# Optimization experiments

Hardware: AMD Instinct MI355X
Metric: run time of the kernel (lower is better)

Reference implementation:

```python
import jax, jax.numpy as jnp
import numpy as np

V, D, H, L, F, S, B = 32000, 1024, 16, 4, 4096, 1024, 2
THETA = 10000.0
EPS = 1e-5


def rmsnorm(x, w):
    # faithful to source: rms = sqrt(mean(x^2)) + eps (eps OUTSIDE the sqrt)
    rms = jnp.sqrt(jnp.mean(x * x, axis=-1, keepdims=True)) + EPS
    return (x / rms) * w


def rope(x, pos):
    # x: [B, H, S, dk]; rotate interleaved even/odd pairs
    dk = x.shape[-1]
    inv_freq = 1.0 / (THETA ** (jnp.arange(0, dk, 2, dtype=jnp.float32) / dk))
    ang = pos[:, None].astype(jnp.float32) * inv_freq[None, :]  # [S, dk/2]
    cos, sin = jnp.cos(ang), jnp.sin(ang)
    x1, x2 = x[..., ::2], x[..., 1::2]
    r1 = x1 * cos - x2 * sin
    r2 = x1 * sin + x2 * cos
    return jnp.stack([r1, r2], axis=-1).reshape(x.shape)


def setup_inputs() -> dict:
    key = jax.random.key(0)
    ks = jax.random.split(key, 12)
    s_attn = np.sqrt(2.0 / (D + D)).astype(np.float32)
    s_ffn = np.sqrt(2.0 / (F + D)).astype(np.float32)
    s_head = np.sqrt(2.0 / (V + D)).astype(np.float32)
    return {
        "token_ids": jax.random.randint(ks[0], (B, S), 0, V),
        "tok_emb": jax.random.normal(ks[1], (V, D), jnp.float32),
        "lm_head_w": jax.random.normal(ks[2], (V, D), jnp.float32) * s_head,
        "ln_final_w": jnp.ones((D,), jnp.float32),
        "q_w": jax.random.normal(ks[3], (L, D, D), jnp.float32) * s_attn,
        "k_w": jax.random.normal(ks[4], (L, D, D), jnp.float32) * s_attn,
        "v_w": jax.random.normal(ks[5], (L, D, D), jnp.float32) * s_attn,
        "o_w": jax.random.normal(ks[6], (L, D, D), jnp.float32) * s_attn,
        "ln1_w": jnp.ones((L, D), jnp.float32),
        "ln2_w": jnp.ones((L, D), jnp.float32),
        "w1": jax.random.normal(ks[7], (L, F, D), jnp.float32) * s_ffn,
        "w2": jax.random.normal(ks[8], (L, D, F), jnp.float32) * s_ffn,
        "w3": jax.random.normal(ks[9], (L, F, D), jnp.float32) * s_ffn,
    }


def reference(token_ids, tok_emb, lm_head_w, ln_final_w, q_w, k_w, v_w, o_w,
              ln1_w, ln2_w, w1, w2, w3):
    b, s = token_ids.shape
    dk = D // H
    scale = 1.0 / np.sqrt(dk).astype(np.float32)
    pos = jnp.arange(s)
    causal = jnp.tril(jnp.ones((s, s), dtype=bool))  # mask[i,j] = i >= j
    x = tok_emb[token_ids]  # [B, S, D]

    for l in range(L):
        # attention block with RoPE
        h = rmsnorm(x, ln1_w[l])
        q = (h @ q_w[l].T).reshape(b, s, H, dk).transpose(0, 2, 1, 3)
        k = (h @ k_w[l].T).reshape(b, s, H, dk).transpose(0, 2, 1, 3)
        v = (h @ v_w[l].T).reshape(b, s, H, dk).transpose(0, 2, 1, 3)
        q = rope(q, pos)
        k = rope(k, pos)
        scores = jnp.einsum('bhqd,bhkd->bhqk', q, k) * scale
        scores = jnp.where(causal, scores, -jnp.inf)
        attn = jax.nn.softmax(scores, axis=-1)
        o = jnp.einsum('bhqk,bhkd->bhqd', attn, v)
        o = o.transpose(0, 2, 1, 3).reshape(b, s, D)
        x = x + o @ o_w[l].T

        # SwiGLU FFN block
        h2 = rmsnorm(x, ln2_w[l])
        xw = h2 @ w1[l].T                       # [B, S, F]
        swish = xw * jax.nn.sigmoid(xw)
        x = x + (swish * (h2 @ w3[l].T)) @ w2[l].T

    x = rmsnorm(x, ln_final_w)
    return x @ lm_head_w.T  # logits [B, S, V]
```

## Files before the change

kernel.cpp:

```cpp
#include <hip/hip_runtime.h>
#include <math.h>

#define V_SZ 32000
#define D_SZ 1024
#define H_SZ 16
#define L_SZ 4
#define F_SZ 4096
#define S_SZ 1024
#define B_SZ 2
#define DK 64
#define NTOK (B_SZ * S_SZ)
#define NEG_INF -3.0e38f

typedef _Float16 half8 __attribute__((ext_vector_type(8)));
typedef _Float16 half4 __attribute__((ext_vector_type(4)));
typedef float floatx4 __attribute__((ext_vector_type(4)));

__device__ __forceinline__ void gload16(const void* g, void* l) {
    __builtin_amdgcn_global_load_lds(
        (const __attribute__((address_space(1))) unsigned int*)g,
        (__attribute__((address_space(3))) unsigned int*)l, 16, 0, 0);
}

__global__ __launch_bounds__(256) void prep1(const float* __restrict__ x,
                                             const float* __restrict__ lnw,
                                             _Float16* __restrict__ hout,
                                             const float* __restrict__ sq,
                                             const float* __restrict__ sk,
                                             const float* __restrict__ sv,
                                             const float* __restrict__ so,
                                             const float* __restrict__ s1,
                                             const float* __restrict__ s3,
                                             const float* __restrict__ s2,
                                             _Float16* __restrict__ d,
                                             int nDD8, int nFD8) {
    const int tid = threadIdx.x;
    if (blockIdx.x < NTOK) {
        const int row = blockIdx.x;
        const float4 v = ((const float4*)(x + (size_t)row * D_SZ))[tid];
        float ss = v.x * v.x + v.y * v.y + v.z * v.z + v.w * v.w;
#pragma unroll
        for (int off = 32; off > 0; off >>= 1) ss += __shfl_down(ss, off, 64);
        __shared__ float red[4];
        if ((tid & 63) == 0) red[tid >> 6] = ss;
        __syncthreads();
        const float tot = red[0] + red[1] + red[2] + red[3];
        const float inv = 1.0f / (sqrtf(tot * (1.0f / (float)D_SZ)) + 1e-5f);
        const float4 wv = ((const float4*)lnw)[tid];
        half4 o = {(_Float16)(v.x * inv * wv.x), (_Float16)(v.y * inv * wv.y),
                   (_Float16)(v.z * inv * wv.z), (_Float16)(v.w * inv * wv.w)};
        ((half4*)(hout + (size_t)row * D_SZ))[tid] = o;
        return;
    }
    const int i = (blockIdx.x - NTOK) * 256 + tid;
    const float* s;
    int off;
    if (i < 4 * nDD8) {
        const int sel = i / nDD8;
        off = i - sel * nDD8;
        s = sel == 0 ? sq : (sel == 1 ? sk : (sel == 2 ? sv : so));
    } else {
        const int j = i - 4 * nDD8;
        const int sel = j / nFD8;
        off = j - sel * nFD8;
        s = sel == 0 ? s1 : (sel == 1 ? s3 : s2);
    }
    const float4 a = ((const float4*)s)[2 * off];
    const float4 b = ((const float4*)s)[2 * off + 1];
    half8 hv = {(_Float16)a.x, (_Float16)a.y, (_Float16)a.z, (_Float16)a.w,
                (_Float16)b.x, (_Float16)b.y, (_Float16)b.z, (_Float16)b.w};
    ((half8*)d)[i] = hv;
}

__global__ __launch_bounds__(256) void prep2(const float* __restrict__ x,
                                             const float* __restrict__ lnw,
                                             _Float16* __restrict__ hout,
                                             const float* __restrict__ win,
                                             _Float16* __restrict__ wout) {
    const int tid = threadIdx.x;
    if (blockIdx.x < NTOK) {
        const int row = blockIdx.x;
        const float4 v = ((const float4*)(x + (size_t)row * D_SZ))[tid];
        float ss = v.x * v.x + v.y * v.y + v.z * v.z + v.w * v.w;
#pragma unroll
        for (int off = 32; off > 0; off >>= 1) ss += __shfl_down(ss, off, 64);
        __shared__ float red[4];
        if ((tid & 63) == 0) red[tid >> 6] = ss;
        __syncthreads();
        const float tot = red[0] + red[1] + red[2] + red[3];
        const float inv = 1.0f / (sqrtf(tot * (1.0f / (float)D_SZ)) + 1e-5f);
        const float4 wv = ((const float4*)lnw)[tid];
        half4 o = {(_Float16)(v.x * inv * wv.x), (_Float16)(v.y * inv * wv.y),
                   (_Float16)(v.z * inv * wv.z), (_Float16)(v.w * inv * wv.w)};
        ((half4*)(hout + (size_t)row * D_SZ))[tid] = o;
        return;
    }
    const int i = (blockIdx.x - NTOK) * 256 + tid;
    const float4 a = ((const float4*)win)[2 * i];
    const float4 b = ((const float4*)win)[2 * i + 1];
    half8 hv = {(_Float16)a.x, (_Float16)a.y, (_Float16)a.z, (_Float16)a.w,
                (_Float16)b.x, (_Float16)b.y, (_Float16)b.z, (_Float16)b.w};
    ((half8*)wout)[i] = hv;
}

__global__ __launch_bounds__(256) void embed_kernel(const int* __restrict__ ids,
                                                    const float* __restrict__ emb,
                                                    float* __restrict__ x) {
    const int row = blockIdx.x;
    const int id = ids[row];
    const float4* src = (const float4*)(emb + (size_t)id * D_SZ);
    float4* dst = (float4*)(x + (size_t)row * D_SZ);
    dst[threadIdx.x] = src[threadIdx.x];
}

__global__ __launch_bounds__(256) void rmsnorm_kernel(const float* __restrict__ x,
                                                      const float* __restrict__ w,
                                                      _Float16* __restrict__ out) {
    const int row = blockIdx.x;
    const int tid = threadIdx.x;
    const float4 v = ((const float4*)(x + (size_t)row * D_SZ))[tid];
    float ss = v.x * v.x + v.y * v.y + v.z * v.z + v.w * v.w;
#pragma unroll
    for (int off = 32; off > 0; off >>= 1) ss += __shfl_down(ss, off, 64);
    __shared__ float red[4];
    if ((tid & 63) == 0) red[tid >> 6] = ss;
    __syncthreads();
    const float tot = red[0] + red[1] + red[2] + red[3];
    const float inv = 1.0f / (sqrtf(tot * (1.0f / (float)D_SZ)) + 1e-5f);
    const float4 wv = ((const float4*)w)[tid];
    half4 o = {(_Float16)(v.x * inv * wv.x), (_Float16)(v.y * inv * wv.y),
               (_Float16)(v.z * inv * wv.z), (_Float16)(v.w * inv * wv.w)};
    ((half4*)(out + (size_t)row * D_SZ))[tid] = o;
}

template <bool MFAST>
__global__ __launch_bounds__(512) void hgemm8p(const _Float16* __restrict__ A,
                                               const _Float16* __restrict__ B,
                                               float* __restrict__ Cf,
                                               int M, int N, int K) {
    __shared__ __align__(16) _Float16 As[2][2][256 * 32];
    __shared__ __align__(16) _Float16 Bs[2][2][256 * 32];
    const int tid = threadIdx.x;
    const int lane = tid & 63, wave = tid >> 6;
    const int wm = wave >> 2, wn = wave & 3;
    const int l15 = lane & 15, g = lane >> 4;

    const int gm = M >> 8, gn = N >> 8, nwg = gm * gn;
    const int orig = blockIdx.x;
    const int q8 = nwg >> 3, r8 = nwg & 7, xcd = orig & 7, j8 = orig >> 3;
    const int wgid = (xcd < r8 ? xcd * (q8 + 1) : r8 * (q8 + 1) + (xcd - r8) * q8) + j8;
    const int bm = MFAST ? (wgid % gm) : (wgid / gn);
    const int bn = MFAST ? (wgid / gm) : (wgid % gn);
    const int m0 = bm << 8, n0 = bn << 8;

    const int rowS = tid >> 2;
    const int srcC = ((tid & 3) ^ ((rowS >> 1) & 3)) << 4;
    const size_t Kb = (size_t)K * 2;
    const char* gA = (const char*)A + (size_t)(m0 + rowS) * Kb + srcC;
    const char* gB = (const char*)B + (size_t)(n0 + rowS) * Kb + srcC;
    const size_t g128 = 128 * Kb;

#define STA(ks, t, buf) do {                                              \
        const char* _s = gA + (size_t)(t) * 128 + (ks) * 64;              \
        char* _d = (char*)&As[buf][ks][0];                                \
        gload16(_s, _d + tid * 16);                                       \
        gload16(_s + g128, _d + 8192 + tid * 16);                         \
    } while (0)
#define STB(ks, t, buf) do {                                              \
        const char* _s = gB + (size_t)(t) * 128 + (ks) * 64;              \
        char* _d = (char*)&Bs[buf][ks][0];                                \
        gload16(_s, _d + tid * 16);                                       \
        gload16(_s + g128, _d + 8192 + tid * 16);                         \
    } while (0)

    half8 aF[8], bF[2];
#define READA(buf, ks) do {                                               \
        _Pragma("unroll")                                                 \
        for (int i = 0; i < 8; i++) {                                     \
            const int R = wm * 128 + i * 16 + l15;                        \
            aF[i] = *(const half8*)((const char*)&As[buf][ks][0] +        \
                                    R * 64 + ((g ^ ((R >> 1) & 3)) << 4));\
        }                                                                 \
    } while (0)
#define READB(buf, ks, nh) do {                                           \
        _Pragma("unroll")                                                 \
        for (int jj = 0; jj < 2; jj++) {                                  \
            const int R = wn * 64 + ((nh) * 2 + jj) * 16 + l15;           \
            bF[jj] = *(const half8*)((const char*)&Bs[buf][ks][0] +       \
                                     R * 64 + ((g ^ ((R >> 1) & 3)) << 4));\
        }                                                                 \
    } while (0)
#define MFMA16(nh) do {                                                   \
        __builtin_amdgcn_s_setprio(1);                                    \
        _Pragma("unroll")                                                 \
        for (int i = 0; i < 8; i++) {                                     \
            acc[i][(nh) * 2 + 0] = __builtin_amdgcn_mfma_f32_16x16x32_f16(\
                aF[i], bF[0], acc[i][(nh) * 2 + 0], 0, 0, 0);             \
            acc[i][(nh) * 2 + 1] = __builtin_amdgcn_mfma_f32_16x16x32_f16(\
                aF[i], bF[1], acc[i][(nh) * 2 + 1], 0, 0, 0);             \
        }                                                                 \
        __builtin_amdgcn_s_setprio(0);                                    \
    } while (0)
#define FENCE_MID() do {                                                  \
        __builtin_amdgcn_s_barrier();                                     \
        asm volatile("s_waitcnt lgkmcnt(0)" ::: "memory");                \
        __builtin_amdgcn_sched_barrier(0);                                \
    } while (0)

    floatx4 acc[8][4];
#pragma unroll
    for (int i = 0; i < 8; i++)
#pragma unroll
        for (int j = 0; j < 4; j++) acc[i][j] = 0;

    const int nt = K >> 6;
    STA(0, 0, 0); STB(0, 0, 0); STA(1, 0, 0); STB(1, 0, 0);
    STA(0, 1, 1); STB(0, 1, 1);

    for (int t = 0; t < nt; ++t) {
        const int buf = t & 1, nbuf = buf ^ 1;
        if (t == nt - 1) asm volatile("s_waitcnt vmcnt(0)" ::: "memory");
        else             asm volatile("s_waitcnt vmcnt(4)" ::: "memory");
        __builtin_amdgcn_s_barrier();
        READA(buf, 0); READB(buf, 0, 0);
        if (t + 1 < nt) STA(1, t + 1, nbuf);
        FENCE_MID();
        MFMA16(0);
        __builtin_amdgcn_s_barrier();
        READB(buf, 0, 1);
        if (t + 1 < nt) STB(1, t + 1, nbuf);
        FENCE_MID();
        MFMA16(1);
        __builtin_amdgcn_s_barrier();
        READA(buf, 1); READB(buf, 1, 0);
        if (t + 2 < nt) STA(0, t + 2, buf);
        FENCE_MID();
        MFMA16(0);
        __builtin_amdgcn_s_barrier();
        READB(buf, 1, 1);
        if (t + 2 < nt) STB(0, t + 2, buf);
        FENCE_MID();
        MFMA16(1);
        __builtin_amdgcn_s_barrier();
    }
#undef STA
#undef STB
#undef READA
#undef READB
#undef MFMA16
#undef FENCE_MID

#pragma unroll
    for (int i = 0; i < 8; i++) {
#pragma unroll
        for (int e = 0; e < 4; e++) {
            const int row = m0 + wm * 128 + i * 16 + g * 4 + e;
#pragma unroll
            for (int j = 0; j < 4; j++) {
                const int col = n0 + wn * 64 + j * 16 + l15;
                Cf[(size_t)row * N + col] = acc[i][j][e];
            }
        }
    }
}

template <int EPI, bool MFAST, int TM>
__global__ __launch_bounds__(256) void hgemm(const _Float16* __restrict__ A,
                                             const _Float16* __restrict__ B,
                                             float* __restrict__ Cf,
                                             _Float16* Ch,
                                             const _Float16* AUXh,
                                             _Float16* Cq,
                                             _Float16* Ck,
                                             _Float16* Cv,
                                             int M, int N, int K) {
    constexpr int WN = (TM == 128) ? 2 : 4;
    constexpr int CW = 128 / WN;
    constexpr int FN = CW / 16;
    __shared__ __align__(16) _Float16 As[2][TM * 32];
    __shared__ __align__(16) _Float16 Bs[2][128 * 32];
    const int tid = threadIdx.x;
    const int lane = tid & 63;
    const int wave = tid >> 6;
    const int wr = (TM == 128) ? (wave >> 1) : 0;
    const int wc = (TM == 128) ? (wave & 1) : wave;
    const int l15 = lane & 15, g = lane >> 4;

    const int gm = M / TM, gn = N >> 7, nwg = gm * gn;
    const int orig = blockIdx.x;
    const int q8 = nwg >> 3, r8 = nwg & 7, xcd = orig & 7, j8 = orig >> 3;
    const int wgid = (xcd < r8 ? xcd * (q8 + 1) : r8 * (q8 + 1) + (xcd - r8) * q8) + j8;
    const int bm = MFAST ? (wgid % gm) : (wgid / gn);
    const int bn = MFAST ? (wgid / gm) : (wgid % gn);
    const int m0 = bm * TM, n0 = bn * 128;

    const int offA0 = wave * (TM * 16) + lane * 16;
    const int offA1 = offA0 + 1024;
    const int rA0 = offA0 >> 6, kA0 = offA0 & 63;
    const int rA1 = offA1 >> 6, kA1 = offA1 & 63;
    const int offB0 = wave * 2048 + lane * 16;
    const int offB1 = offB0 + 1024;
    const int rB0 = offB0 >> 6, kB0 = offB0 & 63;
    const int rB1 = offB1 >> 6, kB1 = offB1 & 63;
    const char* gA0 = (const char*)(A + (size_t)(m0 + rA0) * K) + kA0;
    const char* gA1 = (const char*)(A + (size_t)(m0 + rA1) * K) + kA1;
    const char* gB0 = (const char*)(B + (size_t)(n0 + rB0) * K) + kB0;
    const char* gB1 = (const char*)(B + (size_t)(n0 + rB1) * K) + kB1;

#define STAGE(buf)                                                     \
    do {                                                               \
        gload16(gA0, (char*)As[buf] + offA0);                          \
        if constexpr (TM == 128) gload16(gA1, (char*)As[buf] + offA1); \
        gload16(gB0, (char*)Bs[buf] + offB0);                          \
        gload16(gB1, (char*)Bs[buf] + offB1);                          \
        gA0 += 64; gA1 += 64; gB0 += 64; gB1 += 64;                    \
    } while (0)

    floatx4 acc[4][FN];
#pragma unroll
    for (int i = 0; i < 4; i++)
#pragma unroll
        for (int j = 0; j < FN; j++) acc[i][j] = 0;

    STAGE(0);
    __syncthreads();
    int cur = 0;
    for (int kk = 0; kk < K; kk += 32) {
        if (kk + 32 < K) STAGE(cur ^ 1);
        half8 aF[4], bF[FN];
#pragma unroll
        for (int i = 0; i < 4; i++)
            aF[i] = *(const half8*)&As[cur][(wr * 64 + i * 16 + l15) * 32 + g * 8];
#pragma unroll
        for (int j = 0; j < FN; j++)
            bF[j] = *(const half8*)&Bs[cur][(wc * CW + j * 16 + l15) * 32 + g * 8];
#pragma unroll
        for (int i = 0; i < 4; i++)
#pragma unroll
            for (int j = 0; j < FN; j++)
                acc[i][j] = __builtin_amdgcn_mfma_f32_16x16x32_f16(aF[i], bF[j], acc[i][j], 0, 0, 0);
        __syncthreads();
        cur ^= 1;
    }
#undef STAGE

    const int rb = m0 + wr * 64 + g * 4;
    const int cb = n0 + wc * CW + l15;
    if (EPI == 4) {
        const int sel = n0 >> 10;
        _Float16* Cx = sel == 0 ? Cq : (sel == 1 ? Ck : Cv);
        const int cb0 = cb - sel * 1024;
#pragma unroll
        for (int i = 0; i < 4; i++) {
#pragma unroll
            for (int e = 0; e < 4; e++) {
                const int row = rb + i * 16 + e;
                const int pos = row & (S_SZ - 1);
#pragma unroll
                for (int j = 0; j < FN; j++) {
                    float v = acc[i][j][e];
                    const int col = cb0 + j * 16;
                    if (sel < 2) {
                        const float pp = __shfl_xor(v, 1, 64);
                        const int pi = (col & 63) >> 1;
                        const float invf = exp2f((float)pi * -0.41524101186f);
                        float sn, cs;
                        sincosf((float)pos * invf, &sn, &cs);
                        v = (col & 1) ? (pp * sn + v * cs) : (v * cs - pp * sn);
                    }
                    Cx[(size_t)row * 1024 + col] = (_Float16)v;
                }
            }
        }
        return;
    }
#pragma unroll
    for (int i = 0; i < 4; i++) {
#pragma unroll
        for (int e = 0; e < 4; e++) {
            const int row = rb + i * 16 + e;
#pragma unroll
            for (int j = 0; j < FN; j++) {
                const float v = acc[i][j][e];
                const int col = cb + j * 16;
                if (EPI == 0) {
                    Cf[(size_t)row * N + col] = v;
                } else if (EPI == 1) {
                    Cf[(size_t)row * N + col] += v;
                } else if (EPI == 2) {
                    Ch[(size_t)row * N + col] =
                        (_Float16)(v / (1.0f + __expf(-v)));
                } else if (EPI == 3) {
                    const size_t idx = (size_t)row * N + col;
                    Ch[idx] = (_Float16)((float)AUXh[idx] * v);
                }
            }
        }
    }
}

__global__ __launch_bounds__(256) void hgemm_ff(const _Float16* __restrict__ A,
                                                const _Float16* __restrict__ B1,
                                                const _Float16* __restrict__ B3,
                                                _Float16* __restrict__ Ch,
                                                int M, int N, int K) {
    __shared__ __align__(16) _Float16 As[2][64 * 32];
    __shared__ __align__(16) _Float16 Bs1[2][128 * 32];
    __shared__ __align__(16) _Float16 Bs3[2][128 * 32];
    const int tid = threadIdx.x;
    const int lane = tid & 63;
    const int wave = tid >> 6;
    const int l15 = lane & 15, g = lane >> 4;

    const int gm = M >> 6, gn = N >> 7, nwg = gm * gn;
    const int orig = blockIdx.x;
    const int q8 = nwg >> 3, r8 = nwg & 7, xcd = orig & 7, j8 = orig >> 3;
    const int wgid = (xcd < r8 ? xcd * (q8 + 1) : r8 * (q8 + 1) + (xcd - r8) * q8) + j8;
    const int bm = wgid % gm, bn = wgid / gm;
    const int m0 = bm * 64, n0 = bn * 128;

    const int offA = wave * 1024 + lane * 16;
    const int rA = offA >> 6, kA = offA & 63;
    const int offB0 = wave * 2048 + lane * 16;
    const int offB1 = offB0 + 1024;
    const int rB0 = offB0 >> 6, kB0 = offB0 & 63;
    const int rB1 = offB1 >> 6, kB1 = offB1 & 63;
    const char* gA  = (const char*)(A  + (size_t)(m0 + rA) * K) + kA;
    const char* gB10 = (const char*)(B1 + (size_t)(n0 + rB0) * K) + kB0;
    const char* gB11 = (const char*)(B1 + (size_t)(n0 + rB1) * K) + kB1;
    const char* gB30 = (const char*)(B3 + (size_t)(n0 + rB0) * K) + kB0;
    const char* gB31 = (const char*)(B3 + (size_t)(n0 + rB1) * K) + kB1;

#define STAGEF(buf)                                   \
    do {                                              \
        gload16(gA,   (char*)As[buf]  + offA);        \
        gload16(gB10, (char*)Bs1[buf] + offB0);       \
        gload16(gB11, (char*)Bs1[buf] + offB1);       \
        gload16(gB30, (char*)Bs3[buf] + offB0);       \
        gload16(gB31, (char*)Bs3[buf] + offB1);       \
        gA += 64; gB10 += 64; gB11 += 64;             \
        gB30 += 64; gB31 += 64;                       \
    } while (0)

    floatx4 acc1[4][2], acc3[4][2];
#pragma unroll
    for (int i = 0; i < 4; i++)
#pragma unroll
        for (int j = 0; j < 2; j++) { acc1[i][j] = 0; acc3[i][j] = 0; }

    STAGEF(0);
    __syncthreads();
    int cur = 0;
    for (int kk = 0; kk < K; kk += 32) {
        if (kk + 32 < K) STAGEF(cur ^ 1);
        half8 aF[4], b1F[2], b3F[2];
#pragma unroll
        for (int i = 0; i < 4; i++)
            aF[i] = *(const half8*)&As[cur][(i * 16 + l15) * 32 + g * 8];
#pragma unroll
        for (int j = 0; j < 2; j++) {
            b1F[j] = *(const half8*)&Bs1[cur][(wave * 32 + j * 16 + l15) * 32 + g * 8];
            b3F[j] = *(const half8*)&Bs3[cur][(wave * 32 + j * 16 + l15) * 32 + g * 8];
        }
#pragma unroll
        for (int i = 0; i < 4; i++)
#pragma unroll
            for (int j = 0; j < 2; j++) {
                acc1[i][j] = __builtin_amdgcn_mfma_f32_16x16x32_f16(aF[i], b1F[j], acc1[i][j], 0, 0, 0);
                acc3[i][j] = __builtin_amdgcn_mfma_f32_16x16x32_f16(aF[i], b3F[j], acc3[i][j], 0, 0, 0);
            }
        __syncthreads();
        cur ^= 1;
    }
#undef STAGEF

    const int cb = n0 + wave * 32 + l15;
#pragma unroll
    for (int i = 0; i < 4; i++) {
#pragma unroll
        for (int e = 0; e < 4; e++) {
            const int row = m0 + i * 16 + g * 4 + e;
#pragma unroll
            for (int j = 0; j < 2; j++) {
                const float v1 = acc1[i][j][e];
                const float v3 = acc3[i][j][e];
                const float sw = v1 / (1.0f + __expf(-v1));
                Ch[(size_t)row * N + cb + j * 16] = (_Float16)(sw * v3);
            }
        }
    }
}

__global__ __launch_bounds__(256) void vtrans(const _Float16* __restrict__ vh,
                                              _Float16* __restrict__ vt) {
    __shared__ __align__(16) _Float16 Ls[64][80];
    const int t = threadIdx.x;
    const int s0 = blockIdx.x * 64;
    const int bh = blockIdx.y;
    const int b = bh >> 4, h = bh & 15;
#pragma unroll
    for (int p = 0; p < 2; ++p) {
        const int sl = p * 32 + (t >> 3);
        const int d = (t & 7) * 8;
        *(half8*)&Ls[sl][d] =
            *(const half8*)&vh[((size_t)b * S_SZ + s0 + sl) * D_SZ + h * 64 + d];
    }
    __syncthreads();
#pragma unroll
    for (int p = 0; p < 2; ++p) {
        const int d = p * 32 + (t >> 3);
        const int sc = (t & 7) * 8;
        half8 v;
#pragma unroll
        for (int j = 0; j < 8; ++j) v[j] = Ls[sc + j][d];
        *(half8*)&vt[((size_t)bh * 64 + d) * S_SZ + s0 + sc] = v;
    }
}

__global__ __launch_bounds__(256) void attn_split(const _Float16* __restrict__ qh,
                                                  const _Float16* __restrict__ kh,
                                                  const _Float16* __restrict__ vt,
                                                  _Float16* __restrict__ aop,
                                                  float2* __restrict__ ml) {
    __shared__ __align__(16) _Float16 Ks[2][64 * 64];
    __shared__ __align__(16) _Float16 Vs[2][64 * 64];
    __shared__ __align__(16) _Float16 Ps[4][16][88];
    const int tid = threadIdx.x;
    const int lane = tid & 63, wave = tid >> 6;
    const int l15 = lane & 15, g = lane >> 4;
    const int bx = blockIdx.x;
    const int bh = blockIdx.y;
    const int par = blockIdx.z;
    const int h = bh & 15;
    const size_t tokb = (size_t)(bh >> 4) * S_SZ;

    const int qt0 = bx, qt1 = 15 - bx;
    const int qb0 = qt0 * 64, qb1 = qt1 * 64;
    const int ktmax = qt1;

    const int qrow = l15 * 4 + wave;
    half8 qA0[2], qA1[2];
#pragma unroll
    for (int kk = 0; kk < 2; ++kk) {
        qA0[kk] = *(const half8*)&qh[(tokb + qb0 + qrow) * D_SZ + h * 64 + kk * 32 + g * 8];
        qA1[kk] = *(const half8*)&qh[(tokb + qb1 + qrow) * D_SZ + h * 64 + kk * 32 + g * 8];
    }

    floatx4 accO0[4], accO1[4];
#pragma unroll
    for (int s = 0; s < 4; s++) { accO0[s] = 0; accO1[s] = 0; }
    float m0_[4] = {NEG_INF, NEG_INF, NEG_INF, NEG_INF};
    float l0_[4] = {0.0f, 0.0f, 0.0f, 0.0f};
    float m1_[4] = {NEG_INF, NEG_INF, NEG_INF, NEG_INF};
    float l1_[4] = {0.0f, 0.0f, 0.0f, 0.0f};

    const char* KbB = (const char*)(kh + tokb * D_SZ + h * 64);
    const char* VbB = (const char*)(vt + (size_t)bh * 64 * S_SZ);
    const int so0 = wave * 2048 + lane * 16;
    const int so1 = so0 + 1024;
    const int r0 = so0 >> 7, c0 = (so0 >> 4) & 7;
    const int r1 = so1 >> 7, c1 = (so1 >> 4) & 7;
    const int gc0 = ((c0 ^ (r0 & 7)) << 4);
    const int gc1 = ((c1 ^ (r1 & 7)) << 4);

#define STAGEKV(buf, kt)                                                   \
    do {                                                                   \
        const size_t kvr = (size_t)(kt) * 64;                              \
        gload16(KbB + (kvr + r0) * 2048 + gc0, (char*)Ks[buf] + so0);      \
        gload16(KbB + (kvr + r1) * 2048 + gc1, (char*)Ks[buf] + so1);      \
        gload16(VbB + r0 * 2048 + kvr * 2 + gc0, (char*)Vs[buf] + so0);    \
        gload16(VbB + r1 * 2048 + kvr * 2 + gc1, (char*)Vs[buf] + so1);    \
    } while (0)

#define LDSW(arr, rr, cc) \
    (*(const half8*)&(arr)[(rr) * 64 + ((((cc) ^ ((rr) & 7))) << 3)])

    auto computeTile = [&](const half8* qA, floatx4* accO, float* m_, float* l_,
                           int qbase, int kt, bool diag, int buf) {
        const int kv0 = kt * 64;
        floatx4 accS[4];
        __builtin_amdgcn_s_setprio(1);
#pragma unroll
        for (int sub = 0; sub < 4; ++sub) {
            accS[sub] = 0;
#pragma unroll
            for (int kk = 0; kk < 2; ++kk) {
                half8 kB = LDSW(Ks[buf], sub * 16 + l15, kk * 4 + g);
                accS[sub] = __builtin_amdgcn_mfma_f32_16x16x32_f16(qA[kk], kB, accS[sub], 0, 0, 0);
            }
        }
        __builtin_amdgcn_s_setprio(0);
        float sv[4][4];
        float mx[4] = {NEG_INF, NEG_INF, NEG_INF, NEG_INF};
#pragma unroll
        for (int sub = 0; sub < 4; ++sub)
#pragma unroll
            for (int e = 0; e < 4; ++e) {
                float s = accS[sub][e] * 0.125f;
                if (diag && (kv0 + sub * 16 + l15 > qbase + (g * 4 + e) * 4 + wave))
                    s = NEG_INF;
                sv[sub][e] = s;
                mx[e] = fmaxf(mx[e], s);
            }
#pragma unroll
        for (int msk = 1; msk <= 8; msk <<= 1)
#pragma unroll
            for (int e = 0; e < 4; ++e)
                mx[e] = fmaxf(mx[e], __shfl_xor(mx[e], msk, 64));
        float sf[4];
#pragma unroll
        for (int e = 0; e < 4; ++e) {
            const float mn = fmaxf(m_[e], mx[e]);
            sf[e] = __expf(m_[e] - mn);
            m_[e] = mn;
        }
        float rs[4] = {0.0f, 0.0f, 0.0f, 0.0f};
#pragma unroll
        for (int sub = 0; sub < 4; ++sub)
#pragma unroll
            for (int e = 0; e < 4; ++e) {
                const float p = __expf(sv[sub][e] - m_[e]);
                sv[sub][e] = p;
                rs[e] += p;
            }
#pragma unroll
        for (int msk = 1; msk <= 8; msk <<= 1)
#pragma unroll
            for (int e = 0; e < 4; ++e)
                rs[e] += __shfl_xor(rs[e], msk, 64);
#pragma unroll
        for (int e = 0; e < 4; ++e) l_[e] = l_[e] * sf[e] + rs[e];
#pragma unroll
        for (int sub = 0; sub < 4; ++sub)
#pragma unroll
            for (int e = 0; e < 4; ++e) accO[sub][e] *= sf[e];
#pragma unroll
        for (int sub = 0; sub < 4; ++sub)
#pragma unroll
            for (int e = 0; e < 4; ++e)
                Ps[wave][g * 4 + e][sub * 16 + l15] = (_Float16)sv[sub][e];
        half8 aP[2];
        aP[0] = *(const half8*)&Ps[wave][l15][g * 8];
        aP[1] = *(const half8*)&Ps[wave][l15][32 + g * 8];
        __builtin_amdgcn_s_setprio(1);
#pragma unroll
        for (int sub = 0; sub < 4; ++sub)
#pragma unroll
            for (int kk = 0; kk < 2; ++kk) {
                half8 vB = LDSW(Vs[buf], sub * 16 + l15, kk * 4 + g);
                accO[sub] = __builtin_amdgcn_mfma_f32_16x16x32_f16(aP[kk], vB, accO[sub], 0, 0, 0);
            }
        __builtin_amdgcn_s_setprio(0);
    };

    STAGEKV(0, par);
    __syncthreads();
    int cur = 0;
    for (int kt = par; kt <= ktmax; kt += 2) {
        if (kt + 2 <= ktmax) STAGEKV(cur ^ 1, kt + 2);
        computeTile(qA1, accO1, m1_, l1_, qb1, kt, kt == qt1, cur);
        if (kt <= qt0)
            computeTile(qA0, accO0, m0_, l0_, qb0, kt, kt == qt0, cur);
        __syncthreads();
        cur ^= 1;
    }
#undef STAGEKV
#undef LDSW

    _Float16* op = aop + (size_t)par * ((size_t)NTOK * D_SZ);
    float2* mlp = ml + (size_t)par * (B_SZ * H_SZ * S_SZ);
#pragma unroll
    for (int e = 0; e < 4; ++e) {
        const int rr = (g * 4 + e) * 4 + wave;
        const float i1 = l1_[e] > 0.0f ? 1.0f / l1_[e] : 0.0f;
        const float i0 = l0_[e] > 0.0f ? 1.0f / l0_[e] : 0.0f;
#pragma unroll
        for (int sub = 0; sub < 4; ++sub) {
            op[(tokb + qb1 + rr) * D_SZ + h * 64 + sub * 16 + l15] =
                (_Float16)(accO1[sub][e] * i1);
            op[(tokb + qb0 + rr) * D_SZ + h * 64 + sub * 16 + l15] =
                (_Float16)(accO0[sub][e] * i0);
        }
        if (l15 == 0) {
            mlp[bh * S_SZ + qb1 + rr] = float2{m1_[e], l1_[e]};
            mlp[bh * S_SZ + qb0 + rr] = float2{m0_[e], l0_[e]};
        }
    }
}

__global__ __launch_bounds__(256) void attn_merge(const _Float16* __restrict__ aop,
                                                  const float2* __restrict__ ml,
                                                  _Float16* __restrict__ ao) {
    const int row = blockIdx.x;
    const int t = threadIdx.x;
    const int col = t * 4;
    const int h = col >> 6;
    const int b = row >> 10, s = row & (S_SZ - 1);
    const int bh = b * H_SZ + h;
    const float2 v0 = ml[bh * S_SZ + s];
    const float2 v1 = ml[B_SZ * H_SZ * S_SZ + bh * S_SZ + s];
    const float m = fmaxf(v0.x, v1.x);
    const float w0 = v0.y * __expf(v0.x - m);
    const float w1 = v1.y * __expf(v1.x - m);
    const float inv = 1.0f / (w0 + w1);
    const float a0 = w0 * inv, a1 = w1 * inv;
    const size_t base = (size_t)row * D_SZ + col;
    const half4 x0 = *(const half4*)(aop + base);
    const half4 x1 = *(const half4*)(aop + (size_t)NTOK * D_SZ + base);
    half4 o;
#pragma unroll
    for (int j = 0; j < 4; ++j)
        o[j] = (_Float16)(a0 * (float)x0[j] + a1 * (float)x1[j]);
    *(half4*)(ao + base) = o;
}

extern "C" void kernel_launch(void* const* d_in, const int* in_sizes, int n_in,
                              void* d_out, int out_size, void* d_ws, size_t ws_size,
                              hipStream_t stream) {
    const int*   token_ids  = (const int*)d_in[0];
    const float* tok_emb    = (const float*)d_in[1];
    const float* lm_head_w  = (const float*)d_in[2];
    const float* ln_final_w = (const float*)d_in[3];
    const float* q_w        = (const float*)d_in[4];
    const float* k_w        = (const float*)d_in[5];
    const float* v_w        = (const float*)d_in[6];
    const float* o_w        = (const float*)d_in[7];
    const float* ln1_w      = (const float*)d_in[8];
    const float* ln2_w      = (const float*)d_in[9];
    const float* w1         = (const float*)d_in[10];
    const float* w2         = (const float*)d_in[11];
    const float* w3         = (const float*)d_in[12];
    float* out = (float*)d_out;

    char* W = (char*)d_ws;
    const size_t MB = 1u << 20;
    float*    x    = (float*)(W + 0);
    _Float16* h    = (_Float16*)(W + 8 * MB);
    _Float16* ao   = (_Float16*)(W + 12 * MB);
    _Float16* wq   = (_Float16*)(W + 16 * MB);
    _Float16* wo   = wq + 3 * (1u << 20);
    _Float16* ww1  = (_Float16*)(W + 24 * MB);
    _Float16* ww3  = ww1 + (size_t)F_SZ * D_SZ;
    _Float16* ww2  = ww1 + 2 * (size_t)F_SZ * D_SZ;
    _Float16* qh   = (_Float16*)(W + 48 * MB);
    _Float16* kh   = (_Float16*)(W + 52 * MB);
    _Float16* vh   = (_Float16*)(W + 56 * MB);
    _Float16* vt   = (_Float16*)(W + 60 * MB);
    _Float16* ff1h = (_Float16*)(W + 64 * MB);
    _Float16* aop  = (_Float16*)(W + 64 * MB);
    float2*   ml   = (float2*)(W + 72 * MB);
    _Float16* whead = (_Float16*)(W + 24 * MB);

    embed_kernel<<<NTOK, 256, 0, stream>>>(token_ids, tok_emb, x);

    const int nDD8 = D_SZ * D_SZ / 8;
    const int nFD8 = F_SZ * D_SZ / 8;
    const int nCNV = 4 * nDD8 + 3 * nFD8;
    const dim3 gPRE1(NTOK + nCNV / 256);
    const dim3 gQKV(3 * D_SZ / 128 * (NTOK / 128));
    const dim3 gD64(D_SZ / 128 * (NTOK / 64));
    const dim3 gFF(F_SZ / 128 * (NTOK / 64));
    const dim3 gATT(S_SZ / 128, B_SZ * H_SZ, 2);
    const dim3 gVT(S_SZ / 64, B_SZ * H_SZ);

    for (int l = 0; l < L_SZ; l++) {
        const size_t oDD = (size_t)l * D_SZ * D_SZ;
        const size_t oFD = (size_t)l * F_SZ * D_SZ;
        prep1<<<gPRE1, 256, 0, stream>>>(x, ln1_w + (size_t)l * D_SZ, h,
                                         q_w + oDD, k_w + oDD, v_w + oDD, o_w + oDD,
                                         w1 + oFD, w3 + oFD, w2 + oFD,
                                         wq, nDD8, nFD8);
        hgemm<4, true, 128><<<gQKV, 256, 0, stream>>>(h, wq, nullptr, nullptr, nullptr,
                                                      qh, kh, vh, NTOK, 3 * D_SZ, D_SZ);
        vtrans<<<gVT, 256, 0, stream>>>(vh, vt);
        attn_split<<<gATT, 256, 0, stream>>>(qh, kh, vt, aop, ml);
        attn_merge<<<NTOK, 256, 0, stream>>>(aop, ml, ao);
        hgemm<1, false, 64><<<gD64, 256, 0, stream>>>(ao, wo, x, nullptr, nullptr,
                                                      nullptr, nullptr, nullptr, NTOK, D_SZ, D_SZ);
        rmsnorm_kernel<<<NTOK, 256, 0, stream>>>(x, ln2_w + (size_t)l * D_SZ, h);
        hgemm_ff<<<gFF, 256, 0, stream>>>(h, ww1, ww3, ff1h, NTOK, F_SZ, D_SZ);
        hgemm<1, false, 64><<<gD64, 256, 0, stream>>>(ff1h, ww2, x, nullptr, nullptr,
                                                      nullptr, nullptr, nullptr, NTOK, D_SZ, F_SZ);
    }
    const int nVD8 = V_SZ * D_SZ / 8;
    prep2<<<NTOK + nVD8 / 256, 256, 0, stream>>>(x, ln_final_w, h, lm_head_w, whead);
    const dim3 gOUT(V_SZ / 256 * (NTOK / 256));
    hgemm8p<true><<<gOUT, 512, 0, stream>>>(h, whead, out, NTOK, V_SZ, D_SZ);
}
```

Before: 1.182 ms.

## Split-K residual GEMMs with atomics, fuse V transpose into QKV epilogue

The two residual-add GEMMs (o_proj and w2) now use split-K=2 with atomicAdd into the fp32 residual, doubling the number of workgroups. The QKV GEMM epilogue writes V directly in transposed [b,h,d,s] layout, which removes the separate vtrans kernel and its round trip through memory. The QKV GEMM also moves from 128-row to 64-row tiles to get more workgroups. The costs are float atomic traffic, nondeterministic summation order, and strided scattered stores for V.

```diff
diff --git a/kernel.cpp b/kernel.cpp
--- a/kernel.cpp
+++ b/kernel.cpp
@@ -264,7 +264,7 @@
     }
 }
 
-template <int EPI, bool MFAST, int TM>
+template <int EPI, bool MFAST, int TM, int SPLITK>
 __global__ __launch_bounds__(256) void hgemm(const _Float16* __restrict__ A,
                                              const _Float16* __restrict__ B,
                                              float* __restrict__ Cf,
@@ -286,13 +286,17 @@
     const int wc = (TM == 128) ? (wave & 1) : wave;
     const int l15 = lane & 15, g = lane >> 4;
 
-    const int gm = M / TM, gn = N >> 7, nwg = gm * gn;
+    const int gm = M / TM, gn = N >> 7, nwgT = gm * gn * SPLITK;
     const int orig = blockIdx.x;
-    const int q8 = nwg >> 3, r8 = nwg & 7, xcd = orig & 7, j8 = orig >> 3;
+    const int q8 = nwgT >> 3, r8 = nwgT & 7, xcd = orig & 7, j8 = orig >> 3;
     const int wgid = (xcd < r8 ? xcd * (q8 + 1) : r8 * (q8 + 1) + (xcd - r8) * q8) + j8;
-    const int bm = MFAST ? (wgid % gm) : (wgid / gn);
-    const int bn = MFAST ? (wgid / gm) : (wgid % gn);
+    const int sk = wgid % SPLITK;
+    const int tile = wgid / SPLITK;
+    const int bm = MFAST ? (tile % gm) : (tile / gn);
+    const int bn = MFAST ? (tile / gm) : (tile % gn);
     const int m0 = bm * TM, n0 = bn * 128;
+    const int Kh = K / SPLITK;
+    const int kOff = sk * Kh * 2;
 
     const int offA0 = wave * (TM * 16) + lane * 16;
     const int offA1 = offA0 + 1024;
@@ -302,10 +306,10 @@
     const int offB1 = offB0 + 1024;
     const int rB0 = offB0 >> 6, kB0 = offB0 & 63;
     const int rB1 = offB1 >> 6, kB1 = offB1 & 63;
-    const char* gA0 = (const char*)(A + (size_t)(m0 + rA0) * K) + kA0;
-    const char* gA1 = (const char*)(A + (size_t)(m0 + rA1) * K) + kA1;
-    const char* gB0 = (const char*)(B + (size_t)(n0 + rB0) * K) + kB0;
-    const char* gB1 = (const char*)(B + (size_t)(n0 + rB1) * K) + kB1;
+    const char* gA0 = (const char*)(A + (size_t)(m0 + rA0) * K) + kA0 + kOff;
+    const char* gA1 = (const char*)(A + (size_t)(m0 + rA1) * K) + kA1 + kOff;
+    const char* gB0 = (const char*)(B + (size_t)(n0 + rB0) * K) + kB0 + kOff;
+    const char* gB1 = (const char*)(B + (size_t)(n0 + rB1) * K) + kB1 + kOff;
 
 #define STAGE(buf)                                                     \
     do {                                                               \
@@ -325,8 +329,8 @@
     STAGE(0);
     __syncthreads();
     int cur = 0;
-    for (int kk = 0; kk < K; kk += 32) {
-        if (kk + 32 < K) STAGE(cur ^ 1);
+    for (int kk = 0; kk < Kh; kk += 32) {
+        if (kk + 32 < Kh) STAGE(cur ^ 1);
         half8 aF[4], bF[FN];
 #pragma unroll
         for (int i = 0; i < 4; i++)
@@ -348,7 +352,6 @@
     const int cb = n0 + wc * CW + l15;
     if (EPI == 4) {
         const int sel = n0 >> 10;
-        _Float16* Cx = sel == 0 ? Cq : (sel == 1 ? Ck : Cv);
         const int cb0 = cb - sel * 1024;
 #pragma unroll
         for (int i = 0; i < 4; i++) {
@@ -367,8 +370,12 @@
                         float sn, cs;
                         sincosf((float)pos * invf, &sn, &cs);
                         v = (col & 1) ? (pp * sn + v * cs) : (v * cs - pp * sn);
+                        _Float16* Cx = sel == 0 ? Cq : Ck;
+                        Cx[(size_t)row * 1024 + col] = (_Float16)v;
+                    } else {
+                        Cv[(((size_t)(row >> 10) << 10) + col) * S_SZ +
+                           (row & (S_SZ - 1))] = (_Float16)v;
                     }
-                    Cx[(size_t)row * 1024 + col] = (_Float16)v;
                 }
             }
         }
@@ -386,7 +393,8 @@
                 if (EPI == 0) {
                     Cf[(size_t)row * N + col] = v;
                 } else if (EPI == 1) {
-                    Cf[(size_t)row * N + col] += v;
+                    if (SPLITK > 1) atomicAdd(&Cf[(size_t)row * N + col], v);
+                    else            Cf[(size_t)row * N + col] += v;
                 } else if (EPI == 2) {
                     Ch[(size_t)row * N + col] =
                         (_Float16)(v / (1.0f + __expf(-v)));
@@ -488,32 +496,6 @@
                 Ch[(size_t)row * N + cb + j * 16] = (_Float16)(sw * v3);
             }
         }
-    }
-}
-
-__global__ __launch_bounds__(256) void vtrans(const _Float16* __restrict__ vh,
-                                              _Float16* __restrict__ vt) {
-    __shared__ __align__(16) _Float16 Ls[64][80];
-    const int t = threadIdx.x;
-    const int s0 = blockIdx.x * 64;
-    const int bh = blockIdx.y;
-    const int b = bh >> 4, h = bh & 15;
-#pragma unroll
-    for (int p = 0; p < 2; ++p) {
-        const int sl = p * 32 + (t >> 3);
-        const int d = (t & 7) * 8;
-        *(half8*)&Ls[sl][d] =
-            *(const half8*)&vh[((size_t)b * S_SZ + s0 + sl) * D_SZ + h * 64 + d];
-    }
-    __syncthreads();
-#pragma unroll
-    for (int p = 0; p < 2; ++p) {
-        const int d = p * 32 + (t >> 3);
-        const int sc = (t & 7) * 8;
-        half8 v;
-#pragma unroll
-        for (int j = 0; j < 8; ++j) v[j] = Ls[sc + j][d];
-        *(half8*)&vt[((size_t)bh * 64 + d) * S_SZ + s0 + sc] = v;
     }
 }
 
@@ -744,8 +726,7 @@
     _Float16* ww2  = ww1 + 2 * (size_t)F_SZ * D_SZ;
     _Float16* qh   = (_Float16*)(W + 48 * MB);
     _Float16* kh   = (_Float16*)(W + 52 * MB);
-    _Float16* vh   = (_Float16*)(W + 56 * MB);
-    _Float16* vt   = (_Float16*)(W + 60 * MB);
+    _Float16* vt   = (_Float16*)(W + 56 * MB);
     _Float16* ff1h = (_Float16*)(W + 64 * MB);
     _Float16* aop  = (_Float16*)(W + 64 * MB);
     float2*   ml   = (float2*)(W + 72 * MB);
@@ -757,12 +738,10 @@
     const int nFD8 = F_SZ * D_SZ / 8;
     const int nCNV = 4 * nDD8 + 3 * nFD8;
     const dim3 gPRE1(NTOK + nCNV / 256);
-    const dim3 gQKV(3 * D_SZ / 128 * (NTOK / 128));
-    const dim3 gD64(D_SZ / 128 * (NTOK / 64));
+    const dim3 gQKV(3 * D_SZ / 128 * (NTOK / 64));
+    const dim3 gD64sk(D_SZ / 128 * (NTOK / 64) * 2);
     const dim3 gFF(F_SZ / 128 * (NTOK / 64));
     const dim3 gATT(S_SZ / 128, B_SZ * H_SZ, 2);
-    const dim3 gVT(S_SZ / 64, B_SZ * H_SZ);
-
     for (int l = 0; l < L_SZ; l++) {
         const size_t oDD = (size_t)l * D_SZ * D_SZ;
         const size_t oFD = (size_t)l * F_SZ * D_SZ;
@@ -770,17 +749,16 @@
                                          q_w + oDD, k_w + oDD, v_w + oDD, o_w + oDD,
                                          w1 + oFD, w3 + oFD, w2 + oFD,
                                          wq, nDD8, nFD8);
-        hgemm<4, true, 128><<<gQKV, 256, 0, stream>>>(h, wq, nullptr, nullptr, nullptr,
-                                                      qh, kh, vh, NTOK, 3 * D_SZ, D_SZ);
-        vtrans<<<gVT, 256, 0, stream>>>(vh, vt);
+        hgemm<4, true, 64, 1><<<gQKV, 256, 0, stream>>>(h, wq, nullptr, nullptr, nullptr,
+                                                        qh, kh, vt, NTOK, 3 * D_SZ, D_SZ);
         attn_split<<<gATT, 256, 0, stream>>>(qh, kh, vt, aop, ml);
         attn_merge<<<NTOK, 256, 0, stream>>>(aop, ml, ao);
-        hgemm<1, false, 64><<<gD64, 256, 0, stream>>>(ao, wo, x, nullptr, nullptr,
-                                                      nullptr, nullptr, nullptr, NTOK, D_SZ, D_SZ);
+        hgemm<1, false, 64, 2><<<gD64sk, 256, 0, stream>>>(ao, wo, x, nullptr, nullptr,
+                                                           nullptr, nullptr, nullptr, NTOK, D_SZ, D_SZ);
         rmsnorm_kernel<<<NTOK, 256, 0, stream>>>(x, ln2_w + (size_t)l * D_SZ, h);
         hgemm_ff<<<gFF, 256, 0, stream>>>(h, ww1, ww3, ff1h, NTOK, F_SZ, D_SZ);
-        hgemm<1, false, 64><<<gD64, 256, 0, stream>>>(ff1h, ww2, x, nullptr, nullptr,
-                                                      nullptr, nullptr, nullptr, NTOK, D_SZ, F_SZ);
+        hgemm<1, false, 64, 2><<<gD64sk, 256, 0, stream>>>(ff1h, ww2, x, nullptr, nullptr,
+                                                           nullptr, nullptr, nullptr, NTOK, D_SZ, F_SZ);
     }
     const int nVD8 = V_SZ * D_SZ / 8;
     prep2<<<NTOK + nVD8 / 256, 256, 0, stream>>>(x, ln_final_w, h, lm_head_w, whead);
```

New measurement: 1.055 ms, median of 2. 10.7% less time.
